# Performance work log

Hardware: AMD Instinct MI355X
Metric: run time of the kernel (lower is better)

Reference implementation:

```python
import jax, jax.numpy as jnp
import numpy as np

B, TX, TY, D, H = 8, 128, 128, 512, 512
LN_EPS = 1e-3  # keras LayerNormalization default epsilon


def setup_inputs() -> dict:
    key = jax.random.key(0)
    ks = jax.random.split(key, 6)
    scale = 1.0 / np.sqrt(D)
    return {
        "context": jax.random.normal(ks[0], (B, TX, D), jnp.float32),
        "x": jax.random.normal(ks[1], (B, TY, D), jnp.float32),
        "Wa": jax.random.normal(ks[2], (D, H), jnp.float32) * scale,
        "bWa": jnp.zeros((H,), jnp.float32),
        "Ua": jax.random.normal(ks[3], (D, H), jnp.float32) * scale,
        "bUa": jnp.zeros((H,), jnp.float32),
        "Va": jax.random.normal(ks[4], (H, 1), jnp.float32) * (1.0 / np.sqrt(H)),
        "bVa": jnp.zeros((1,), jnp.float32),
        "gamma": jnp.ones((D,), jnp.float32),
        "beta": jnp.zeros((D,), jnp.float32),
    }


def reference(context, x, Wa, bWa, Ua, bUa, Va, bVa, gamma, beta):
    # context: [B,Tx,D], x: [B,Ty,D]
    Wc = context @ Wa + bWa                      # [B,Tx,H]
    Ux = x @ Ua + bUa                            # [B,Ty,H]
    t = jnp.tanh(Wc[:, None, :, :] + Ux[:, :, None, :])  # [B,Ty,Tx,H]
    scores = jnp.einsum('btxh,h->btx', t, Va[:, 0]) + bVa[0]  # [B,Ty,Tx]
    attn = jax.nn.softmax(scores, axis=-1)
    cv = jnp.einsum('btx,bxd->btd', attn, context)  # [B,Ty,D]
    mean = jnp.mean(cv, axis=-1, keepdims=True)
    var = jnp.mean(jnp.square(cv - mean), axis=-1, keepdims=True)
    cv = (cv - mean) * jax.lax.rsqrt(var + LN_EPS) * gamma + beta
    return cv + x
```

## Files before the change

### kernel.cpp

```cpp
#include <hip/hip_runtime.h>


#define SCALE 2.0f

typedef __attribute__((ext_vector_type(8))) short short8;
typedef float floatx4 __attribute__((ext_vector_type(4)));

__device__ __forceinline__ unsigned short f2bf(float f) {
  union { float f; unsigned u; } c{f};
  unsigned r = (c.u + 0x7FFFu + ((c.u >> 16) & 1u)) >> 16;
  return (unsigned short)r;
}

__global__ __launch_bounds__(256) void prep_transpose(
    const float* __restrict__ Wa, const float* __restrict__ Ua,
    unsigned short* __restrict__ WaT, unsigned short* __restrict__ UaT) {
  const int id = blockIdx.x;
  const float* __restrict__ W = (id & 64) ? Ua : Wa;
  unsigned short* __restrict__ WT = (id & 64) ? UaT : WaT;
  const int tile = id & 63;
  const int k0 = (tile >> 3) * 64;
  const int n0 = (tile & 7) * 64;
  __shared__ float tl[64][65];
  const int t = threadIdx.x;
  const int c = t & 63, r0 = t >> 6;
#pragma unroll
  for (int p = 0; p < 16; p++) {
    const int k = r0 + p * 4;
    tl[k][c] = W[(k0 + k) * 512 + n0 + c];
  }
  __syncthreads();
  const int nl = t >> 2, kc = (t & 3) * 16;
  unsigned short ov[16];
#pragma unroll
  for (int q = 0; q < 16; q++) ov[q] = f2bf(tl[kc + q][nl]);
  *(short8*)&WT[(size_t)(n0 + nl) * 512 + k0 + kc]     = *(short8*)&ov[0];
  *(short8*)&WT[(size_t)(n0 + nl) * 512 + k0 + kc + 8] = *(short8*)&ov[8];
}

__global__ __launch_bounds__(256) void gemm_mfma(
    const float* __restrict__ ctx, const float* __restrict__ xin,
    const unsigned short* __restrict__ WaT, const unsigned short* __restrict__ UaT,
    const float* __restrict__ bWa, const float* __restrict__ bUa,
    float* __restrict__ WcT, float* __restrict__ Ux) {
  const bool second = (blockIdx.z != 0);
  const float* __restrict__ A = second ? xin : ctx;
  const unsigned short* __restrict__ BT = second ? UaT : WaT;
  const int m0 = blockIdx.x * 64, n0 = blockIdx.y * 64;

  __shared__ __align__(16) unsigned short As[64 * 32];
  __shared__ __align__(16) unsigned short Bs[64 * 32];

  const int t = threadIdx.x;
  const int l = t & 63;
  const int sub = t >> 6;
  const int rl = sub * 16 + (l & 15);
  const int kl = (l >> 4) * 8;

  const float* aptr = A + (size_t)(m0 + rl) * 512 + kl;
  const unsigned short* bptr = BT + (size_t)(n0 + rl) * 512 + kl;

  const int lane = t & 63, w = t >> 6;
  const int wrow = w >> 1, wcol = w & 1;

  floatx4 acc[2][2] = {};

  float4 a0 = *(const float4*)(aptr);
  float4 a1 = *(const float4*)(aptr + 4);
  short8 bv = *(const short8*)(bptr);

  for (int kt = 0; kt < 512; kt += 32) {
    short8 av;
    av[0] = (short)f2bf(a0.x); av[1] = (short)f2bf(a0.y);
    av[2] = (short)f2bf(a0.z); av[3] = (short)f2bf(a0.w);
    av[4] = (short)f2bf(a1.x); av[5] = (short)f2bf(a1.y);
    av[6] = (short)f2bf(a1.z); av[7] = (short)f2bf(a1.w);
    ((short8*)As)[t] = av;
    ((short8*)Bs)[t] = bv;
    __syncthreads();
    if (kt + 32 < 512) {
      a0 = *(const float4*)(aptr + kt + 32);
      a1 = *(const float4*)(aptr + kt + 36);
      bv = *(const short8*)(bptr + kt + 32);
    }
    short8 af[2], bf[2];
    af[0] = ((const short8*)As)[(wrow * 2 + 0) * 64 + lane];
    af[1] = ((const short8*)As)[(wrow * 2 + 1) * 64 + lane];
    bf[0] = ((const short8*)Bs)[(wcol * 2 + 0) * 64 + lane];
    bf[1] = ((const short8*)Bs)[(wcol * 2 + 1) * 64 + lane];
#pragma unroll
    for (int i = 0; i < 2; i++)
#pragma unroll
      for (int j = 0; j < 2; j++)
        acc[i][j] = __builtin_amdgcn_mfma_f32_16x16x32_bf16(af[i], bf[j], acc[i][j], 0, 0, 0);
    __syncthreads();
  }

  const int quad = lane >> 4;
  if (!second) {
#pragma unroll
    for (int i = 0; i < 2; i++)
#pragma unroll
      for (int j = 0; j < 2; j++) {
        const int h = n0 + wcol * 32 + j * 16 + (lane & 15);
        const float bias = bWa[h] + bUa[h];
        const int mg0 = m0 + wrow * 32 + i * 16 + quad * 4;
        const int b = mg0 >> 7, tx0 = mg0 & 127;
        float4 o;
        o.x = (acc[i][j][0] + bias) * SCALE;
        o.y = (acc[i][j][1] + bias) * SCALE;
        o.z = (acc[i][j][2] + bias) * SCALE;
        o.w = (acc[i][j][3] + bias) * SCALE;
        *(float4*)&WcT[(size_t)b * 65536 + (size_t)h * 128 + tx0] = o;
      }
  } else {
#pragma unroll
    for (int i = 0; i < 2; i++)
#pragma unroll
      for (int j = 0; j < 2; j++) {
        const int h = n0 + wcol * 32 + j * 16 + (lane & 15);
        const int mg0 = m0 + wrow * 32 + i * 16 + quad * 4;
#pragma unroll
        for (int r = 0; r < 4; r++)
          Ux[(size_t)(mg0 + r) * 512 + h] = acc[i][j][r] * SCALE;
      }
  }
}

__global__ __launch_bounds__(512) void attn2(
    const float* __restrict__ WcT, const float* __restrict__ Ux,
    const float* __restrict__ ctx, const float* __restrict__ xin,
    const float* __restrict__ Va,
    const float* __restrict__ gamma, const float* __restrict__ beta,
    float* __restrict__ out) {
  const int b = blockIdx.y;
  const int ty0 = blockIdx.x * 4;
  const int t = threadIdx.x;
  const int lane = t & 63, wv = t >> 6;

  __shared__ __align__(16) float s_uxp[512][4];
  __shared__ float s_va[512];
  __shared__ float s_part[16][128];
  __shared__ __align__(16) float s_at[128][4];
  __shared__ float s_red[4][2][8];
  __shared__ float s_mv[4][2];

  {
    const float* uxb = Ux + (size_t)(b * 128 + ty0) * 512;
    for (int i = t; i < 2048; i += 512) {
      const int r = i >> 9, h = i & 511;
      s_uxp[h][r] = uxb[i];
    }
    s_va[t] = Va[t];
  }
  __syncthreads();

  const int tx = t & 127, hq = t >> 7;
  {
    const float* wp = WcT + (size_t)b * 65536 + (size_t)hq * 128 * 128 + tx;
    const float* vap = s_va + hq * 128;
    const float4* up = (const float4*)s_uxp + hq * 128;
    float a0 = 0.f, a1 = 0.f, a2 = 0.f, a3 = 0.f;
#pragma unroll 4
    for (int hh = 0; hh < 128; hh++) {
      const float w = wp[(size_t)hh * 128];
      const float4 u = up[hh];
      const float va = vap[hh];
      a0 = fmaf(va, __builtin_amdgcn_rcpf(1.0f + __expf(w + u.x)), a0);
      a1 = fmaf(va, __builtin_amdgcn_rcpf(1.0f + __expf(w + u.y)), a1);
      a2 = fmaf(va, __builtin_amdgcn_rcpf(1.0f + __expf(w + u.z)), a2);
      a3 = fmaf(va, __builtin_amdgcn_rcpf(1.0f + __expf(w + u.w)), a3);
    }
    s_part[hq * 4 + 0][tx] = a0;
    s_part[hq * 4 + 1][tx] = a1;
    s_part[hq * 4 + 2][tx] = a2;
    s_part[hq * 4 + 3][tx] = a3;
  }
  __syncthreads();

  if (wv < 4) {
    const int r = wv;
    float sA = -2.0f * (s_part[r][lane] + s_part[4 + r][lane] +
                        s_part[8 + r][lane] + s_part[12 + r][lane]);
    float sB = -2.0f * (s_part[r][lane + 64] + s_part[4 + r][lane + 64] +
                        s_part[8 + r][lane + 64] + s_part[12 + r][lane + 64]);
    float m = fmaxf(sA, sB);
#pragma unroll
    for (int off = 32; off; off >>= 1) m = fmaxf(m, __shfl_xor(m, off));
    const float eA = __expf(sA - m);
    const float eB = __expf(sB - m);
    float s = eA + eB;
#pragma unroll
    for (int off = 32; off; off >>= 1) s += __shfl_xor(s, off);
    const float inv = __builtin_amdgcn_rcpf(s);
    s_at[lane][r] = eA * inv;
    s_at[lane + 64][r] = eB * inv;
  }
  __syncthreads();

  const int d = t;
  float cv[4] = {0.f, 0.f, 0.f, 0.f};
  {
    const float* cp = ctx + (size_t)b * 65536 + d;
#pragma unroll 4
    for (int x = 0; x < 128; x++) {
      const float c = cp[(size_t)x * 512];
      const float4 at = *(const float4*)s_at[x];
      cv[0] = fmaf(at.x, c, cv[0]);
      cv[1] = fmaf(at.y, c, cv[1]);
      cv[2] = fmaf(at.z, c, cv[2]);
      cv[3] = fmaf(at.w, c, cv[3]);
    }
  }

#pragma unroll
  for (int r = 0; r < 4; r++) {
    float s = cv[r], q = cv[r] * cv[r];
#pragma unroll
    for (int off = 32; off; off >>= 1) {
      s += __shfl_xor(s, off);
      q += __shfl_xor(q, off);
    }
    if (lane == 0) { s_red[r][0][wv] = s; s_red[r][1][wv] = q; }
  }
  __syncthreads();
  if (t < 4) {
    float s = 0.f, q = 0.f;
#pragma unroll
    for (int i = 0; i < 8; i++) { s += s_red[t][0][i]; q += s_red[t][1][i]; }
    const float mean = s * (1.0f / 512.0f);
    const float var = q * (1.0f / 512.0f) - mean * mean;
    s_mv[t][0] = mean;
    s_mv[t][1] = __builtin_amdgcn_rsqf(var + 1e-3f);
  }
  __syncthreads();

  const float g = gamma[d], bb = beta[d];
#pragma unroll
  for (int r = 0; r < 4; r++) {
    const int row = b * 128 + ty0 + r;
    const float xv = xin[(size_t)row * 512 + d];
    out[(size_t)row * 512 + d] = (cv[r] - s_mv[r][0]) * s_mv[r][1] * g + bb + xv;
  }
}

extern "C" void kernel_launch(void* const* d_in, const int* in_sizes, int n_in,
                              void* d_out, int out_size, void* d_ws, size_t ws_size,
                              hipStream_t stream) {
  const float* ctx   = (const float*)d_in[0];
  const float* xin   = (const float*)d_in[1];
  const float* Wa    = (const float*)d_in[2];
  const float* bWa   = (const float*)d_in[3];
  const float* Ua    = (const float*)d_in[4];
  const float* bUa   = (const float*)d_in[5];
  const float* Va    = (const float*)d_in[6];
  const float* gamma = (const float*)d_in[8];
  const float* beta  = (const float*)d_in[9];
  float* out = (float*)d_out;

  char* ws = (char*)d_ws;
  float* WcT = (float*)ws;
  float* Ux  = (float*)(ws + (2u << 20));
  unsigned short* WaT = (unsigned short*)(ws + (4u << 20));
  unsigned short* UaT = (unsigned short*)(ws + (4u << 20) + (512u << 10));

  prep_transpose<<<128, 256, 0, stream>>>(Wa, Ua, WaT, UaT);
  gemm_mfma<<<dim3(16, 8, 2), 256, 0, stream>>>(ctx, xin, WaT, UaT, bWa, bUa, WcT, Ux);
  attn2<<<dim3(32, 8), 512, 0, stream>>>(WcT, Ux, ctx, xin, Va, gamma, beta, out);
}
```

Measured before the change: 119.1 us.

## Halve rows per attention block, split GEMM loads across 512 threads, use exp2

The attention kernel now handles 2 query rows per block instead of 4, which doubles the grid to 512 blocks but also doubles re-reads of WcT and context per batch. The GEMM uses 512 threads: half load and convert A, half load B, and each wave computes two MFMA tiles instead of four. The tanh path folds log2(e) into SCALE so the hardware exp2 replaces __expf. The aim is more parallelism and occupancy, at the cost of more redundant global traffic in the attention stage.

Result: no change. 117.7 us (-1.2%).

```diff
diff --git a/kernel.cpp b/kernel.cpp
--- a/kernel.cpp
+++ b/kernel.cpp
@@ -1,7 +1,7 @@
 #include <hip/hip_runtime.h>
 
 
-#define SCALE 2.0f
+#define SCALE 2.8853900817779268f
 
 typedef __attribute__((ext_vector_type(8))) short short8;
 typedef float floatx4 __attribute__((ext_vector_type(4)));
@@ -38,7 +38,7 @@
   *(short8*)&WT[(size_t)(n0 + nl) * 512 + k0 + kc + 8] = *(short8*)&ov[8];
 }
 
-__global__ __launch_bounds__(256) void gemm_mfma(
+__global__ __launch_bounds__(512) void gemm_mfma(
     const float* __restrict__ ctx, const float* __restrict__ xin,
     const unsigned short* __restrict__ WaT, const unsigned short* __restrict__ UaT,
     const float* __restrict__ bWa, const float* __restrict__ bUa,
@@ -52,104 +52,103 @@
   __shared__ __align__(16) unsigned short Bs[64 * 32];
 
   const int t = threadIdx.x;
-  const int l = t & 63;
-  const int sub = t >> 6;
-  const int rl = sub * 16 + (l & 15);
-  const int kl = (l >> 4) * 8;
+  const bool isA = (t < 256);
+  const int s = isA ? t : (t - 256);
+  const int sl = s & 63, sub = s >> 6;
+  const int rl = sub * 16 + (sl & 15);
+  const int kl = (sl >> 4) * 8;
 
   const float* aptr = A + (size_t)(m0 + rl) * 512 + kl;
   const unsigned short* bptr = BT + (size_t)(n0 + rl) * 512 + kl;
 
   const int lane = t & 63, w = t >> 6;
-  const int wrow = w >> 1, wcol = w & 1;
-
-  floatx4 acc[2][2] = {};
-
-  float4 a0 = *(const float4*)(aptr);
-  float4 a1 = *(const float4*)(aptr + 4);
-  short8 bv = *(const short8*)(bptr);
+  const int wrow = w & 1, wcol = w >> 1;
+
+  floatx4 acc[2] = {};
+
+  float4 a0, a1; short8 bv;
+  if (isA) { a0 = *(const float4*)(aptr); a1 = *(const float4*)(aptr + 4); }
+  else     { bv = *(const short8*)(bptr); }
 
   for (int kt = 0; kt < 512; kt += 32) {
-    short8 av;
-    av[0] = (short)f2bf(a0.x); av[1] = (short)f2bf(a0.y);
-    av[2] = (short)f2bf(a0.z); av[3] = (short)f2bf(a0.w);
-    av[4] = (short)f2bf(a1.x); av[5] = (short)f2bf(a1.y);
-    av[6] = (short)f2bf(a1.z); av[7] = (short)f2bf(a1.w);
-    ((short8*)As)[t] = av;
-    ((short8*)Bs)[t] = bv;
+    if (isA) {
+      short8 av;
+      av[0] = (short)f2bf(a0.x); av[1] = (short)f2bf(a0.y);
+      av[2] = (short)f2bf(a0.z); av[3] = (short)f2bf(a0.w);
+      av[4] = (short)f2bf(a1.x); av[5] = (short)f2bf(a1.y);
+      av[6] = (short)f2bf(a1.z); av[7] = (short)f2bf(a1.w);
+      ((short8*)As)[s] = av;
+    } else {
+      ((short8*)Bs)[s] = bv;
+    }
     __syncthreads();
     if (kt + 32 < 512) {
-      a0 = *(const float4*)(aptr + kt + 32);
-      a1 = *(const float4*)(aptr + kt + 36);
-      bv = *(const short8*)(bptr + kt + 32);
-    }
-    short8 af[2], bf[2];
+      if (isA) {
+        a0 = *(const float4*)(aptr + kt + 32);
+        a1 = *(const float4*)(aptr + kt + 36);
+      } else {
+        bv = *(const short8*)(bptr + kt + 32);
+      }
+    }
+    short8 af[2], bf;
     af[0] = ((const short8*)As)[(wrow * 2 + 0) * 64 + lane];
     af[1] = ((const short8*)As)[(wrow * 2 + 1) * 64 + lane];
-    bf[0] = ((const short8*)Bs)[(wcol * 2 + 0) * 64 + lane];
-    bf[1] = ((const short8*)Bs)[(wcol * 2 + 1) * 64 + lane];
+    bf    = ((const short8*)Bs)[wcol * 64 + lane];
 #pragma unroll
     for (int i = 0; i < 2; i++)
-#pragma unroll
-      for (int j = 0; j < 2; j++)
-        acc[i][j] = __builtin_amdgcn_mfma_f32_16x16x32_bf16(af[i], bf[j], acc[i][j], 0, 0, 0);
+      acc[i] = __builtin_amdgcn_mfma_f32_16x16x32_bf16(af[i], bf, acc[i], 0, 0, 0);
     __syncthreads();
   }
 
   const int quad = lane >> 4;
+  const int h = n0 + wcol * 16 + (lane & 15);
   if (!second) {
-#pragma unroll
-    for (int i = 0; i < 2; i++)
-#pragma unroll
-      for (int j = 0; j < 2; j++) {
-        const int h = n0 + wcol * 32 + j * 16 + (lane & 15);
-        const float bias = bWa[h] + bUa[h];
-        const int mg0 = m0 + wrow * 32 + i * 16 + quad * 4;
-        const int b = mg0 >> 7, tx0 = mg0 & 127;
-        float4 o;
-        o.x = (acc[i][j][0] + bias) * SCALE;
-        o.y = (acc[i][j][1] + bias) * SCALE;
-        o.z = (acc[i][j][2] + bias) * SCALE;
-        o.w = (acc[i][j][3] + bias) * SCALE;
-        *(float4*)&WcT[(size_t)b * 65536 + (size_t)h * 128 + tx0] = o;
-      }
+    const float bias = bWa[h] + bUa[h];
+#pragma unroll
+    for (int i = 0; i < 2; i++) {
+      const int mg0 = m0 + (wrow * 2 + i) * 16 + quad * 4;
+      const int b = mg0 >> 7, tx0 = mg0 & 127;
+      float4 o;
+      o.x = (acc[i][0] + bias) * SCALE;
+      o.y = (acc[i][1] + bias) * SCALE;
+      o.z = (acc[i][2] + bias) * SCALE;
+      o.w = (acc[i][3] + bias) * SCALE;
+      *(float4*)&WcT[(size_t)b * 65536 + (size_t)h * 128 + tx0] = o;
+    }
   } else {
 #pragma unroll
-    for (int i = 0; i < 2; i++)
-#pragma unroll
-      for (int j = 0; j < 2; j++) {
-        const int h = n0 + wcol * 32 + j * 16 + (lane & 15);
-        const int mg0 = m0 + wrow * 32 + i * 16 + quad * 4;
-#pragma unroll
-        for (int r = 0; r < 4; r++)
-          Ux[(size_t)(mg0 + r) * 512 + h] = acc[i][j][r] * SCALE;
-      }
-  }
-}
-
-__global__ __launch_bounds__(512) void attn2(
+    for (int i = 0; i < 2; i++) {
+      const int mg0 = m0 + (wrow * 2 + i) * 16 + quad * 4;
+#pragma unroll
+      for (int r = 0; r < 4; r++)
+        Ux[(size_t)(mg0 + r) * 512 + h] = acc[i][r] * SCALE;
+    }
+  }
+}
+
+__global__ __launch_bounds__(512) void attn3(
     const float* __restrict__ WcT, const float* __restrict__ Ux,
     const float* __restrict__ ctx, const float* __restrict__ xin,
     const float* __restrict__ Va,
     const float* __restrict__ gamma, const float* __restrict__ beta,
     float* __restrict__ out) {
   const int b = blockIdx.y;
-  const int ty0 = blockIdx.x * 4;
+  const int ty0 = blockIdx.x * 2;
   const int t = threadIdx.x;
   const int lane = t & 63, wv = t >> 6;
 
-  __shared__ __align__(16) float s_uxp[512][4];
+  __shared__ __align__(8) float2 s_ux[512];
   __shared__ float s_va[512];
-  __shared__ float s_part[16][128];
-  __shared__ __align__(16) float s_at[128][4];
-  __shared__ float s_red[4][2][8];
-  __shared__ float s_mv[4][2];
+  __shared__ float s_part[8][128];
+  __shared__ __align__(8) float2 s_at[128];
+  __shared__ float s_red[2][2][8];
+  __shared__ float s_mv[2][2];
 
   {
     const float* uxb = Ux + (size_t)(b * 128 + ty0) * 512;
-    for (int i = t; i < 2048; i += 512) {
+    for (int i = t; i < 1024; i += 512) {
       const int r = i >> 9, h = i & 511;
-      s_uxp[h][r] = uxb[i];
+      ((float*)&s_ux[h])[r] = uxb[i];
     }
     s_va[t] = Va[t];
   }
@@ -158,77 +157,70 @@
   const int tx = t & 127, hq = t >> 7;
   {
     const float* wp = WcT + (size_t)b * 65536 + (size_t)hq * 128 * 128 + tx;
-    const float* vap = s_va + hq * 128;
-    const float4* up = (const float4*)s_uxp + hq * 128;
-    float a0 = 0.f, a1 = 0.f, a2 = 0.f, a3 = 0.f;
+    float a0 = 0.f, a1 = 0.f;
 #pragma unroll 4
     for (int hh = 0; hh < 128; hh++) {
       const float w = wp[(size_t)hh * 128];
-      const float4 u = up[hh];
-      const float va = vap[hh];
-      a0 = fmaf(va, __builtin_amdgcn_rcpf(1.0f + __expf(w + u.x)), a0);
-      a1 = fmaf(va, __builtin_amdgcn_rcpf(1.0f + __expf(w + u.y)), a1);
-      a2 = fmaf(va, __builtin_amdgcn_rcpf(1.0f + __expf(w + u.z)), a2);
-      a3 = fmaf(va, __builtin_amdgcn_rcpf(1.0f + __expf(w + u.w)), a3);
-    }
-    s_part[hq * 4 + 0][tx] = a0;
-    s_part[hq * 4 + 1][tx] = a1;
-    s_part[hq * 4 + 2][tx] = a2;
-    s_part[hq * 4 + 3][tx] = a3;
-  }
-  __syncthreads();
-
-  if (wv < 4) {
+      const float2 u = s_ux[hq * 128 + hh];
+      const float va = s_va[hq * 128 + hh];
+      a0 = fmaf(va, __builtin_amdgcn_rcpf(1.0f + __builtin_amdgcn_exp2f(w + u.x)), a0);
+      a1 = fmaf(va, __builtin_amdgcn_rcpf(1.0f + __builtin_amdgcn_exp2f(w + u.y)), a1);
+    }
+    s_part[hq * 2 + 0][tx] = a0;
+    s_part[hq * 2 + 1][tx] = a1;
+  }
+  __syncthreads();
+
+  if (wv < 2) {
     const int r = wv;
-    float sA = -2.0f * (s_part[r][lane] + s_part[4 + r][lane] +
-                        s_part[8 + r][lane] + s_part[12 + r][lane]);
-    float sB = -2.0f * (s_part[r][lane + 64] + s_part[4 + r][lane + 64] +
-                        s_part[8 + r][lane + 64] + s_part[12 + r][lane + 64]);
+    float sA = -2.0f * (s_part[r][lane] + s_part[2 + r][lane] +
+                        s_part[4 + r][lane] + s_part[6 + r][lane]);
+    float sB = -2.0f * (s_part[r][lane + 64] + s_part[2 + r][lane + 64] +
+                        s_part[4 + r][lane + 64] + s_part[6 + r][lane + 64]);
     float m = fmaxf(sA, sB);
 #pragma unroll
     for (int off = 32; off; off >>= 1) m = fmaxf(m, __shfl_xor(m, off));
     const float eA = __expf(sA - m);
     const float eB = __expf(sB - m);
-    float s = eA + eB;
-#pragma unroll
-    for (int off = 32; off; off >>= 1) s += __shfl_xor(s, off);
-    const float inv = __builtin_amdgcn_rcpf(s);
-    s_at[lane][r] = eA * inv;
-    s_at[lane + 64][r] = eB * inv;
+    float sm = eA + eB;
+#pragma unroll
+    for (int off = 32; off; off >>= 1) sm += __shfl_xor(sm, off);
+    const float inv = __builtin_amdgcn_rcpf(sm);
+    ((float*)&s_at[lane])[r] = eA * inv;
+    ((float*)&s_at[lane + 64])[r] = eB * inv;
   }
   __syncthreads();
 
   const int d = t;
-  float cv[4] = {0.f, 0.f, 0.f, 0.f};
+  float cv0 = 0.f, cv1 = 0.f;
   {
     const float* cp = ctx + (size_t)b * 65536 + d;
 #pragma unroll 4
     for (int x = 0; x < 128; x++) {
       const float c = cp[(size_t)x * 512];
-      const float4 at = *(const float4*)s_at[x];
-      cv[0] = fmaf(at.x, c, cv[0]);
-      cv[1] = fmaf(at.y, c, cv[1]);
-      cv[2] = fmaf(at.z, c, cv[2]);
-      cv[3] = fmaf(at.w, c, cv[3]);
-    }
-  }
-
-#pragma unroll
-  for (int r = 0; r < 4; r++) {
-    float s = cv[r], q = cv[r] * cv[r];
+      const float2 at = s_at[x];
+      cv0 = fmaf(at.x, c, cv0);
+      cv1 = fmaf(at.y, c, cv1);
+    }
+  }
+
+#pragma unroll
+  for (int r = 0; r < 2; r++) {
+    const float v = r ? cv1 : cv0;
+    float sm = v, q = v * v;
 #pragma unroll
     for (int off = 32; off; off >>= 1) {
-      s += __shfl_xor(s, off);
+      sm += __shfl_xor(sm, off);
       q += __shfl_xor(q, off);
     }
-    if (lane == 0) { s_red[r][0][wv] = s; s_red[r][1][wv] = q; }
-  }
-  __syncthreads();
-  if (t < 4) {
-    float s = 0.f, q = 0.f;
-#pragma unroll
-    for (int i = 0; i < 8; i++) { s += s_red[t][0][i]; q += s_red[t][1][i]; }
-    const float mean = s * (1.0f / 512.0f);
+    if (lane == 0) { s_red[r][0][wv] = sm; s_red[r][1][wv] = q; }
+  }
+  __syncthreads();
+  if (t < 2) {
+    float sm = 0.f, q = 0.f;
+#pragma unroll
+    for (int i = 0; i < 8; i++) { sm += s_red[t][0][i]; q += s_red[t][1][i]; }
+    const float mean = sm * (1.0f / 512.0f);
     const float var = q * (1.0f / 512.0f) - mean * mean;
     s_mv[t][0] = mean;
     s_mv[t][1] = __builtin_amdgcn_rsqf(var + 1e-3f);
@@ -237,10 +229,11 @@
 
   const float g = gamma[d], bb = beta[d];
 #pragma unroll
-  for (int r = 0; r < 4; r++) {
+  for (int r = 0; r < 2; r++) {
     const int row = b * 128 + ty0 + r;
+    const float v = r ? cv1 : cv0;
     const float xv = xin[(size_t)row * 512 + d];
-    out[(size_t)row * 512 + d] = (cv[r] - s_mv[r][0]) * s_mv[r][1] * g + bb + xv;
+    out[(size_t)row * 512 + d] = (v - s_mv[r][0]) * s_mv[r][1] * g + bb + xv;
   }
 }
 
@@ -265,6 +258,6 @@
   unsigned short* UaT = (unsigned short*)(ws + (4u << 20) + (512u << 10));
 
   prep_transpose<<<128, 256, 0, stream>>>(Wa, Ua, WaT, UaT);
-  gemm_mfma<<<dim3(16, 8, 2), 256, 0, stream>>>(ctx, xin, WaT, UaT, bWa, bUa, WcT, Ux);
-  attn2<<<dim3(32, 8), 512, 0, stream>>>(WcT, Ux, ctx, xin, Va, gamma, beta, out);
-}
+  gemm_mfma<<<dim3(16, 8, 2), 512, 0, stream>>>(ctx, xin, WaT, UaT, bWa, bUa, WcT, Ux);
+  attn3<<<dim3(64, 8), 512, 0, stream>>>(WcT, Ux, ctx, xin, Va, gamma, beta, out);
+}
```
